# Kernel tuning notes

Hardware: AMD Instinct MI355X
Metric: run time of the kernel (lower is better)

Reference implementation:

```python
import jax, jax.numpy as jnp
import numpy as np

TOP_K = 2


def setup_inputs() -> dict:
    key = jax.random.key(0)
    ks = jax.random.split(key, 5)
    B, S, D, F, E = 2, 1024, 1024, 4096, 8
    return {
        "hidden_states": jax.random.normal(ks[0], (B, S, D), jnp.float32),
        "gate_w": jax.random.normal(ks[1], (E, D), jnp.float32) * 0.02,
        "w1": jax.random.normal(ks[2], (E, D, F), jnp.float32) * 0.02,
        "w2": jax.random.normal(ks[3], (E, F, D), jnp.float32) * 0.02,
        "w3": jax.random.normal(ks[4], (E, D, F), jnp.float32) * 0.02,
    }


def reference(hidden_states, gate_w, w1, w2, w3):
    B, S, D = hidden_states.shape
    E = gate_w.shape[0]
    x = hidden_states.reshape(-1, D).astype(jnp.float32)  # [T, D]
    T = x.shape[0]

    # Router: softmax over experts, top-k, renormalize selected weights.
    router_logits = x @ gate_w.T                      # [T, E]
    probs = jax.nn.softmax(router_logits, axis=-1)
    top_w, top_e = jax.lax.top_k(probs, TOP_K)        # [T, K]
    top_w = top_w / jnp.sum(top_w, axis=-1, keepdims=True)

    # Combine weights [T, E]: weight of expert e for token t (0 if not selected).
    combine = jnp.zeros((T, E), jnp.float32).at[jnp.arange(T)[:, None], top_e].add(top_w)

    # Expert SwiGLU FFNs (vectorized over experts; unselected contributions are
    # zeroed by combine weights, matching the gather/scatter math exactly).
    h = jnp.einsum('td,edf->etf', x, w1)              # [E, T, F]
    g = jnp.einsum('td,edf->etf', x, w3)              # [E, T, F]
    y = jnp.einsum('etf,efd->etd', jax.nn.silu(h) * g, w2)  # [E, T, D]

    out = jnp.einsum('etd,te->td', y, combine)        # weighted scatter-combine
    return out.reshape(B, S, D), router_logits
```

## Files before the change

### kernel.cpp

```cpp
#include <hip/hip_runtime.h>
#include <hip/hip_bf16.h>
#include <math.h>

#define T_TOK   2048
#define DDIM    1024
#define FDIM    4096
#define NEXP    8
#define MAXROWS 4608

typedef __bf16          bf16x8 __attribute__((ext_vector_type(8)));
typedef float           f32x4  __attribute__((ext_vector_type(4)));
typedef unsigned short  u16x8  __attribute__((ext_vector_type(8)));

#define LDSP 40
#define FCW  128

static __device__ __forceinline__ unsigned short f2b(float f) {
    __hip_bfloat16 h = __float2bfloat16(f);
    return __builtin_bit_cast(unsigned short, h);
}

static __device__ __forceinline__ void gll16(const unsigned short* g, unsigned short* l) {
    __builtin_amdgcn_global_load_lds(
        (const __attribute__((address_space(1))) unsigned int*)g,
        (__attribute__((address_space(3))) unsigned int*)l, 16, 0, 0);
}

__global__ __launch_bounds__(256) void moe_router_kernel(
    const float* __restrict__ x, const float* __restrict__ gate_w,
    float* __restrict__ logits_out, int* __restrict__ top_e, float* __restrict__ top_w)
{
    int wid  = (blockIdx.x * blockDim.x + threadIdx.x) >> 6;
    int lane = threadIdx.x & 63;
    if (wid >= T_TOK) return;
    const float* xr = x + (size_t)wid * DDIM;
    float acc[NEXP];
    #pragma unroll
    for (int e = 0; e < NEXP; ++e) acc[e] = 0.f;
    for (int d = lane; d < DDIM; d += 64) {
        float xv = xr[d];
        #pragma unroll
        for (int e = 0; e < NEXP; ++e) acc[e] += xv * gate_w[e * DDIM + d];
    }
    #pragma unroll
    for (int e = 0; e < NEXP; ++e) {
        #pragma unroll
        for (int off = 32; off > 0; off >>= 1)
            acc[e] += __shfl_down(acc[e], off, 64);
    }
    if (lane == 0) {
        #pragma unroll
        for (int e = 0; e < NEXP; ++e) logits_out[wid * NEXP + e] = acc[e];
        int e1 = 0;
        #pragma unroll
        for (int e = 1; e < NEXP; ++e) if (acc[e] > acc[e1]) e1 = e;
        int e2 = (e1 == 0) ? 1 : 0;
        #pragma unroll
        for (int e = 0; e < NEXP; ++e) if (e != e1 && acc[e] > acc[e2]) e2 = e;
        float p2 = __expf(acc[e2] - acc[e1]);
        float s  = 1.0f + p2;
        top_e[wid * 2]     = e1;
        top_e[wid * 2 + 1] = e2;
        top_w[wid * 2]     = 1.0f / s;
        top_w[wid * 2 + 1] = p2 / s;
    }
}

__global__ void moe_scatter_kernel(const int* __restrict__ top_e, const float* __restrict__ top_w,
                                   int* __restrict__ cnt, int* __restrict__ list_tok,
                                   float* __restrict__ list_w)
{
    int t = blockIdx.x * blockDim.x + threadIdx.x;
    if (t >= T_TOK) return;
    #pragma unroll
    for (int s = 0; s < 2; ++s) {
        int e   = top_e[t * 2 + s];
        int pos = atomicAdd(&cnt[e], 1);
        list_tok[e * T_TOK + pos] = t;
        list_w [e * T_TOK + pos] = top_w[t * 2 + s];
    }
}

__global__ void moe_prefix_kernel(const int* __restrict__ cnt, int* __restrict__ offs)
{
    if (threadIdx.x == 0 && blockIdx.x == 0) {
        int o = 0;
        #pragma unroll
        for (int e = 0; e < NEXP; ++e) { offs[e] = o; o += ((cnt[e] + 63) >> 6) << 6; }
        offs[NEXP] = o;
    }
}

__global__ __launch_bounds__(256) void transpose_cvt2_kernel(
    const float* __restrict__ srcA, unsigned short* __restrict__ dstA,
    const float* __restrict__ srcB, unsigned short* __restrict__ dstB, int R, int C)
{
    int tilesC = C >> 6;
    int tilesPerMat = (R >> 6) * tilesC;
    int e  = blockIdx.x / tilesPerMat;
    int t  = blockIdx.x - e * tilesPerMat;
    int tr = t / tilesC, tc = t - tr * tilesC;
    size_t soff = (size_t)e * R * C + (size_t)(tr * 64) * C + tc * 64;
    size_t doff = (size_t)e * R * C + (size_t)(tc * 64) * R + tr * 64;

    __shared__ unsigned short lds[64][72];
    int tid = threadIdx.x;
    int rr = tid >> 4, cc = (tid & 15) * 4;
    int orow = tid >> 2, oc = (tid & 3) * 16;

    #pragma unroll
    for (int m = 0; m < 2; ++m) {
        const float*    s = (m == 0 ? srcA : srcB) + soff;
        unsigned short* d = (m == 0 ? dstA : dstB) + doff;
        if (m) __syncthreads();
        #pragma unroll
        for (int i = 0; i < 4; ++i) {
            int r = rr + 16 * i;
            float4 v = *(const float4*)(s + (size_t)r * C + cc);
            lds[cc + 0][r] = f2b(v.x); lds[cc + 1][r] = f2b(v.y);
            lds[cc + 2][r] = f2b(v.z); lds[cc + 3][r] = f2b(v.w);
        }
        __syncthreads();
        u16x8 a = *(const u16x8*)&lds[orow][oc];
        u16x8 b = *(const u16x8*)&lds[orow][oc + 8];
        *(u16x8*)(d + (size_t)orow * R + oc)     = a;
        *(u16x8*)(d + (size_t)orow * R + oc + 8) = b;
    }
}

__global__ __launch_bounds__(256) void transpose_cvt_kernel(
    const float* __restrict__ src, unsigned short* __restrict__ dst, int R, int C)
{
    int tilesC = C >> 6;
    int tilesPerMat = (R >> 6) * tilesC;
    int e  = blockIdx.x / tilesPerMat;
    int t  = blockIdx.x - e * tilesPerMat;
    int tr = t / tilesC, tc = t - tr * tilesC;
    const float*    s = src + (size_t)e * R * C + (size_t)(tr * 64) * C + tc * 64;
    unsigned short* d = dst + (size_t)e * R * C + (size_t)(tc * 64) * R + tr * 64;

    __shared__ unsigned short lds[64][72];
    int tid = threadIdx.x;
    int rr = tid >> 4, cc = (tid & 15) * 4;
    #pragma unroll
    for (int i = 0; i < 4; ++i) {
        int r = rr + 16 * i;
        float4 v = *(const float4*)(s + (size_t)r * C + cc);
        lds[cc + 0][r] = f2b(v.x); lds[cc + 1][r] = f2b(v.y);
        lds[cc + 2][r] = f2b(v.z); lds[cc + 3][r] = f2b(v.w);
    }
    __syncthreads();
    int orow = tid >> 2, oc = (tid & 3) * 16;
    u16x8 a = *(const u16x8*)&lds[orow][oc];
    u16x8 b = *(const u16x8*)&lds[orow][oc + 8];
    *(u16x8*)(d + (size_t)orow * R + oc)     = a;
    *(u16x8*)(d + (size_t)orow * R + oc + 8) = b;
}

__global__ __launch_bounds__(256) void moe_gather_kernel(
    const float* __restrict__ x, const int* __restrict__ list_tok,
    const int* __restrict__ cnt, const int* __restrict__ offs,
    unsigned short* __restrict__ xg)
{
    int e  = blockIdx.x >> 8;
    int rb = blockIdx.x & 255;
    int n = cnt[e];
    int npad = (n + 63) & ~63;
    if (rb * 8 >= npad) return;
    int base = offs[e];
    int tid = threadIdx.x;
    #pragma unroll
    for (int i = 0; i < 4; ++i) {
        int u = tid + 256 * i;
        int r = u >> 7, cu = u & 127;
        int slot = rb * 8 + r;
        int tok = list_tok[e * T_TOK + slot];
        const float* sp = x + (size_t)tok * DDIM + cu * 8;
        float4 v0 = *(const float4*)(sp);
        float4 v1 = *(const float4*)(sp + 4);
        u16x8 t8;
        t8[0]=f2b(v0.x); t8[1]=f2b(v0.y); t8[2]=f2b(v0.z); t8[3]=f2b(v0.w);
        t8[4]=f2b(v1.x); t8[5]=f2b(v1.y); t8[6]=f2b(v1.z); t8[7]=f2b(v1.w);
        *(u16x8*)(xg + (size_t)(base + slot) * DDIM + cu * 8) = t8;
    }
}

__global__ __launch_bounds__(256, 3) void moe_up_kernel(
    const unsigned short* __restrict__ xg,
    const unsigned short* __restrict__ w1t, const unsigned short* __restrict__ w3t,
    const int* __restrict__ cnt, const int* __restrict__ offs,
    unsigned short* __restrict__ act)
{
    int e   = blockIdx.x & 7;
    int idx = blockIdx.x >> 3;
    int mt  = idx >> 6;
    int fc  = idx & 63;
    int n = cnt[e];
    int npad = (n + 63) & ~63;
    if (mt * 128 >= npad) return;
    int rowBase  = offs[e] + mt * 128;
    int rowMax   = offs[e] + npad - 1;
    int rowLimit = offs[e] + npad;

    __shared__ unsigned short As [128 * 32];
    __shared__ unsigned short B1s[64 * 32];
    __shared__ unsigned short B2s[64 * 32];

    int tid = threadIdx.x;
    int lane = tid & 63, wv = tid >> 6;
    int c = lane & 15, g = lane >> 4;
    int wr = (wv >> 1) * 64, wc = (wv & 1) * 32;

    int srow = tid >> 2, skc = tid & 3;
    int r0 = min(rowBase + srow,      rowMax);
    int r1 = min(rowBase + 64 + srow, rowMax);
    const unsigned short* gA0 = xg + (size_t)r0 * DDIM + skc * 8;
    const unsigned short* gA1 = xg + (size_t)r1 * DDIM + skc * 8;
    size_t wb = (size_t)e * FDIM * DDIM + (size_t)(fc * 64 + srow) * DDIM + skc * 8;
    const unsigned short* gB1 = w1t + wb;
    const unsigned short* gB2 = w3t + wb;
    unsigned short* lA0 = As  + tid * 8;
    unsigned short* lA1 = As  + 2048 + tid * 8;
    unsigned short* lB1 = B1s + tid * 8;
    unsigned short* lB2 = B2s + tid * 8;

    f32x4 acc_h[4][2], acc_g[4][2];
    #pragma unroll
    for (int i = 0; i < 4; ++i)
        #pragma unroll
        for (int j = 0; j < 2; ++j) { acc_h[i][j] = (f32x4)(0.f); acc_g[i][j] = (f32x4)(0.f); }

    for (int k0 = 0; k0 < DDIM; k0 += 32) {
        gll16(gA0 + k0, lA0);
        gll16(gA1 + k0, lA1);
        gll16(gB1 + k0, lB1);
        gll16(gB2 + k0, lB2);
        __syncthreads();

        bf16x8 af[4];
        #pragma unroll
        for (int mi = 0; mi < 4; ++mi)
            af[mi] = *reinterpret_cast<const bf16x8*>(&As[(wr + mi * 16 + c) * 32 + g * 8]);
        #pragma unroll
        for (int ni = 0; ni < 2; ++ni) {
            bf16x8 b1 = *reinterpret_cast<const bf16x8*>(&B1s[(wc + ni * 16 + c) * 32 + g * 8]);
            bf16x8 b2 = *reinterpret_cast<const bf16x8*>(&B2s[(wc + ni * 16 + c) * 32 + g * 8]);
            #pragma unroll
            for (int mi = 0; mi < 4; ++mi) {
                acc_h[mi][ni] = __builtin_amdgcn_mfma_f32_16x16x32_bf16(af[mi], b1, acc_h[mi][ni], 0, 0, 0);
                acc_g[mi][ni] = __builtin_amdgcn_mfma_f32_16x16x32_bf16(af[mi], b2, acc_g[mi][ni], 0, 0, 0);
            }
        }
        __syncthreads();
    }

    #pragma unroll
    for (int mi = 0; mi < 4; ++mi) {
        int row = rowBase + wr + mi * 16 + 4 * g;
        if (row < rowLimit) {
            #pragma unroll
            for (int ni = 0; ni < 2; ++ni) {
                int col = fc * 64 + wc + ni * 16 + c;
                #pragma unroll
                for (int r = 0; r < 4; ++r) {
                    float h  = acc_h[mi][ni][r];
                    float gg = acc_g[mi][ni][r];
                    float a  = h / (1.f + __expf(-h)) * gg;
                    act[(size_t)(row + r) * FDIM + col] = f2b(a);
                }
            }
        }
    }
}

__global__ __launch_bounds__(256, 4) void moe_down_kernel(
    const unsigned short* __restrict__ act, const unsigned short* __restrict__ w2t,
    const int* __restrict__ cnt, const int* __restrict__ offs,
    const int* __restrict__ list_tok, const float* __restrict__ list_w,
    float* __restrict__ out)
{
    int e   = blockIdx.x & 7;
    int idx = blockIdx.x >> 3;
    int mt  = idx >> 5;
    int ks  = (idx >> 4) & 1;
    int dc  = idx & 15;
    int n = cnt[e];
    int npad = (n + 63) & ~63;
    if (mt * 128 >= npad) return;
    int rowBase = offs[e] + mt * 128;
    int rowMax  = offs[e] + npad - 1;

    __shared__ unsigned short As[128 * 32];
    __shared__ unsigned short Bs[64 * 32];

    int tid = threadIdx.x;
    int lane = tid & 63, wv = tid >> 6;
    int c = lane & 15, g = lane >> 4;
    int wr = (wv >> 1) * 64, wc = (wv & 1) * 32;

    int srow = tid >> 2, skc = tid & 3;
    int r0 = min(rowBase + srow,      rowMax);
    int r1 = min(rowBase + 64 + srow, rowMax);
    const unsigned short* gA0 = act + (size_t)r0 * FDIM + ks * 2048 + skc * 8;
    const unsigned short* gA1 = act + (size_t)r1 * FDIM + ks * 2048 + skc * 8;
    const unsigned short* gB  = w2t + (size_t)e * DDIM * FDIM
                                    + (size_t)(dc * 64 + srow) * FDIM + ks * 2048 + skc * 8;
    unsigned short* lA0 = As + tid * 8;
    unsigned short* lA1 = As + 2048 + tid * 8;
    unsigned short* lB  = Bs + tid * 8;

    f32x4 acc[4][2];
    #pragma unroll
    for (int i = 0; i < 4; ++i)
        #pragma unroll
        for (int j = 0; j < 2; ++j) acc[i][j] = (f32x4)(0.f);

    for (int k0 = 0; k0 < 2048; k0 += 32) {
        gll16(gA0 + k0, lA0);
        gll16(gA1 + k0, lA1);
        gll16(gB  + k0, lB);
        __syncthreads();

        bf16x8 af[4];
        #pragma unroll
        for (int mi = 0; mi < 4; ++mi)
            af[mi] = *reinterpret_cast<const bf16x8*>(&As[(wr + mi * 16 + c) * 32 + g * 8]);
        #pragma unroll
        for (int ni = 0; ni < 2; ++ni) {
            bf16x8 b = *reinterpret_cast<const bf16x8*>(&Bs[(wc + ni * 16 + c) * 32 + g * 8]);
            #pragma unroll
            for (int mi = 0; mi < 4; ++mi)
                acc[mi][ni] = __builtin_amdgcn_mfma_f32_16x16x32_bf16(af[mi], b, acc[mi][ni], 0, 0, 0);
        }
        __syncthreads();
    }

    #pragma unroll
    for (int mi = 0; mi < 4; ++mi) {
        #pragma unroll
        for (int r = 0; r < 4; ++r) {
            int s = mt * 128 + wr + mi * 16 + 4 * g + r;
            if (s < n) {
                int   tok = list_tok[e * T_TOK + s];
                float wt  = list_w [e * T_TOK + s];
                #pragma unroll
                for (int ni = 0; ni < 2; ++ni) {
                    int col = dc * 64 + wc + ni * 16 + c;
                    atomicAdd(&out[(size_t)tok * DDIM + col], wt * acc[mi][ni][r]);
                }
            }
        }
    }
}

__global__ __launch_bounds__(256, 3) void moe_up_legacy(
    const float* __restrict__ x, const float* __restrict__ w1, const float* __restrict__ w3,
    const int* __restrict__ cnt, const int* __restrict__ offs,
    const int* __restrict__ list_tok, unsigned short* __restrict__ act)
{
    const int NWG = NEXP * 32 * 32;
    int bid     = blockIdx.x;
    int logical = (bid & 7) * (NWG >> 3) + (bid >> 3);
    int tile = logical & 31;
    int fc   = (logical >> 5) & 31;
    int e    = logical >> 10;
    int n = cnt[e];
    if (tile * 64 >= n) return;

    __shared__ unsigned short As [64  * LDSP];
    __shared__ unsigned short B1s[FCW * LDSP];
    __shared__ unsigned short B2s[FCW * LDSP];

    int tid = threadIdx.x;
    int lane = tid & 63, wv = tid >> 6;
    int c = lane & 15, g = lane >> 4;
    int ar = tid >> 2, akq = tid & 3;
    int tok = list_tok[e * T_TOK + tile * 64 + ar];
    const float* xrow = x + (size_t)tok * DDIM + akq * 8;
    int bcol = tid & 127, bkh = tid >> 7;
    const size_t wbase = (size_t)e * DDIM * FDIM + (size_t)fc * FCW + bcol;
    const float* w1c = w1 + wbase;
    const float* w3c = w3 + wbase;

    f32x4 acc_h[4][2], acc_g[4][2];
    #pragma unroll
    for (int i = 0; i < 4; ++i)
        #pragma unroll
        for (int j = 0; j < 2; ++j) { acc_h[i][j] = (f32x4)(0.f); acc_g[i][j] = (f32x4)(0.f); }

    for (int k0 = 0; k0 < DDIM; k0 += 32) {
        {
            const float4 v0 = *(const float4*)(xrow + k0);
            const float4 v1 = *(const float4*)(xrow + k0 + 4);
            u16x8 t8;
            t8[0]=f2b(v0.x); t8[1]=f2b(v0.y); t8[2]=f2b(v0.z); t8[3]=f2b(v0.w);
            t8[4]=f2b(v1.x); t8[5]=f2b(v1.y); t8[6]=f2b(v1.z); t8[7]=f2b(v1.w);
            *reinterpret_cast<u16x8*>(&As[ar * LDSP + akq * 8]) = t8;
        }
        {
            int kb = k0 + bkh * 16;
            u16x8 t1a, t1b, t2a, t2b;
            #pragma unroll
            for (int j = 0; j < 8; ++j) {
                t1a[j] = f2b(w1c[(size_t)(kb + j)     * FDIM]);
                t1b[j] = f2b(w1c[(size_t)(kb + 8 + j) * FDIM]);
                t2a[j] = f2b(w3c[(size_t)(kb + j)     * FDIM]);
                t2b[j] = f2b(w3c[(size_t)(kb + 8 + j) * FDIM]);
            }
            *reinterpret_cast<u16x8*>(&B1s[bcol * LDSP + bkh * 16])     = t1a;
            *reinterpret_cast<u16x8*>(&B1s[bcol * LDSP + bkh * 16 + 8]) = t1b;
            *reinterpret_cast<u16x8*>(&B2s[bcol * LDSP + bkh * 16])     = t2a;
            *reinterpret_cast<u16x8*>(&B2s[bcol * LDSP + bkh * 16 + 8]) = t2b;
        }
        __syncthreads();
        bf16x8 af[4];
        #pragma unroll
        for (int mi = 0; mi < 4; ++mi)
            af[mi] = *reinterpret_cast<const bf16x8*>(&As[(mi * 16 + c) * LDSP + g * 8]);
        #pragma unroll
        for (int ni = 0; ni < 2; ++ni) {
            int col = wv * 32 + ni * 16 + c;
            bf16x8 b1 = *reinterpret_cast<const bf16x8*>(&B1s[col * LDSP + g * 8]);
            bf16x8 b2 = *reinterpret_cast<const bf16x8*>(&B2s[col * LDSP + g * 8]);
            #pragma unroll
            for (int mi = 0; mi < 4; ++mi) {
                acc_h[mi][ni] = __builtin_amdgcn_mfma_f32_16x16x32_bf16(af[mi], b1, acc_h[mi][ni], 0, 0, 0);
                acc_g[mi][ni] = __builtin_amdgcn_mfma_f32_16x16x32_bf16(af[mi], b2, acc_g[mi][ni], 0, 0, 0);
            }
        }
        __syncthreads();
    }
    int rowBase = offs[e] + tile * 64;
    #pragma unroll
    for (int mi = 0; mi < 4; ++mi)
        #pragma unroll
        for (int ni = 0; ni < 2; ++ni)
            #pragma unroll
            for (int r = 0; r < 4; ++r) {
                float h  = acc_h[mi][ni][r];
                float gg = acc_g[mi][ni][r];
                float a  = h / (1.f + __expf(-h)) * gg;
                int row = rowBase + mi * 16 + 4 * g + r;
                int col = fc * FCW + wv * 32 + ni * 16 + c;
                act[(size_t)row * FDIM + col] = f2b(a);
            }
}

__global__ __launch_bounds__(256, 3) void moe_down_legacy(
    const unsigned short* __restrict__ act, const float* __restrict__ w2,
    const int* __restrict__ cnt, const int* __restrict__ offs,
    const int* __restrict__ list_tok, const float* __restrict__ list_w,
    float* __restrict__ out)
{
    const int NWG = NEXP * 4 * 4 * 32;
    int bid     = blockIdx.x;
    int logical = (bid & 7) * (NWG >> 3) + (bid >> 3);
    int tile = logical & 31;
    int ks   = (logical >> 5) & 3;
    int dc   = (logical >> 7) & 3;
    int e    = logical >> 9;
    int n = cnt[e];
    if (tile * 64 >= n) return;

    __shared__ unsigned short As[64  * LDSP];
    __shared__ unsigned short Bs[256 * LDSP];
    int tid = threadIdx.x;
    int lane = tid & 63, wv = tid >> 6;
    int c = lane & 15, g = lane >> 4;
    int rowBase = offs[e] + tile * 64;
    int ar = tid >> 2, akq = tid & 3;
    const unsigned short* arow = act + (size_t)(rowBase + ar) * FDIM + ks * 1024 + akq * 8;
    const float* w2c = w2 + (size_t)e * FDIM * DDIM + (size_t)(ks * 1024) * DDIM + (size_t)dc * 256 + tid;

    f32x4 acc[4][4];
    #pragma unroll
    for (int i = 0; i < 4; ++i)
        #pragma unroll
        for (int j = 0; j < 4; ++j) acc[i][j] = (f32x4)(0.f);

    for (int k0 = 0; k0 < 1024; k0 += 32) {
        *reinterpret_cast<u16x8*>(&As[ar * LDSP + akq * 8]) = *reinterpret_cast<const u16x8*>(arow + k0);
        #pragma unroll
        for (int kk = 0; kk < 4; ++kk) {
            u16x8 t1;
            #pragma unroll
            for (int j = 0; j < 8; ++j)
                t1[j] = f2b(w2c[(size_t)(k0 + kk * 8 + j) * DDIM]);
            *reinterpret_cast<u16x8*>(&Bs[tid * LDSP + kk * 8]) = t1;
        }
        __syncthreads();
        bf16x8 af[4];
        #pragma unroll
        for (int mi = 0; mi < 4; ++mi)
            af[mi] = *reinterpret_cast<const bf16x8*>(&As[(mi * 16 + c) * LDSP + g * 8]);
        #pragma unroll
        for (int ni = 0; ni < 4; ++ni) {
            bf16x8 b = *reinterpret_cast<const bf16x8*>(&Bs[(wv * 64 + ni * 16 + c) * LDSP + g * 8]);
            #pragma unroll
            for (int mi = 0; mi < 4; ++mi)
                acc[mi][ni] = __builtin_amdgcn_mfma_f32_16x16x32_bf16(af[mi], b, acc[mi][ni], 0, 0, 0);
        }
        __syncthreads();
    }
    #pragma unroll
    for (int mi = 0; mi < 4; ++mi)
        #pragma unroll
        for (int r = 0; r < 4; ++r) {
            int s = tile * 64 + mi * 16 + 4 * g + r;
            if (s < n) {
                int   tok = list_tok[e * T_TOK + s];
                float wt  = list_w [e * T_TOK + s];
                #pragma unroll
                for (int ni = 0; ni < 4; ++ni) {
                    int col = dc * 256 + wv * 64 + ni * 16 + c;
                    atomicAdd(&out[(size_t)tok * DDIM + col], wt * acc[mi][ni][r]);
                }
            }
        }
}

extern "C" void kernel_launch(void* const* d_in, const int* in_sizes, int n_in,
                              void* d_out, int out_size, void* d_ws, size_t ws_size,
                              hipStream_t stream) {
    const float* x      = (const float*)d_in[0];
    const float* gate_w = (const float*)d_in[1];
    const float* w1     = (const float*)d_in[2];
    const float* w2     = (const float*)d_in[3];
    const float* w3     = (const float*)d_in[4];
    float* out        = (float*)d_out;
    float* logits_out = out + (size_t)T_TOK * DDIM;

    char* ws = (char*)d_ws;
    int*   cnt      = (int*)  (ws);
    int*   offs     = (int*)  (ws + 64);
    int*   top_e    = (int*)  (ws + 1024);
    float* top_w    = (float*)(ws + 17408);
    int*   list_tok = (int*)  (ws + 33792);
    float* list_w   = (float*)(ws + 99328);

    hipMemsetAsync(cnt, 0, 64, stream);
    hipMemsetAsync(list_tok, 0, 131072, stream);
    hipMemsetAsync(out, 0, (size_t)T_TOK * DDIM * sizeof(float), stream);

    moe_router_kernel <<<T_TOK / 4,   256, 0, stream>>>(x, gate_w, logits_out, top_e, top_w);
    moe_scatter_kernel<<<T_TOK / 256, 256, 0, stream>>>(top_e, top_w, cnt, list_tok, list_w);
    moe_prefix_kernel <<<1, 64, 0, stream>>>(cnt, offs);

    const size_t MB = 1u << 20;
    const size_t NEED = 241 * MB;
    if (ws_size >= NEED) {
        unsigned short* xg  = (unsigned short*)(ws + 1   * MB);
        unsigned short* act = (unsigned short*)(ws + 11  * MB);
        unsigned short* w1t = (unsigned short*)(ws + 49  * MB);
        unsigned short* w3t = (unsigned short*)(ws + 113 * MB);
        unsigned short* w2t = (unsigned short*)(ws + 177 * MB);

        moe_gather_kernel<<<NEXP * 256, 256, 0, stream>>>(x, list_tok, cnt, offs, xg);
        transpose_cvt2_kernel<<<NEXP * 16 * 64, 256, 0, stream>>>(w1, w1t, w3, w3t, DDIM, FDIM);
        transpose_cvt_kernel <<<NEXP * 64 * 16, 256, 0, stream>>>(w2, w2t, FDIM, DDIM);

        moe_up_kernel   <<<NEXP * 16 * 64, 256, 0, stream>>>(xg, w1t, w3t, cnt, offs, act);
        moe_down_kernel <<<NEXP * 16 * 32, 256, 0, stream>>>(act, w2t, cnt, offs, list_tok, list_w, out);
    } else {
        unsigned short* act = (unsigned short*)(ws + 164864);
        moe_up_legacy   <<<NEXP * 32 * 32,    256, 0, stream>>>(x, w1, w3, cnt, offs, list_tok, act);
        moe_down_legacy <<<NEXP * 4 * 4 * 32, 256, 0, stream>>>(act, w2, cnt, offs, list_tok, list_w, out);
    }
}
```

Before: 355.7 us.

## Fuse weight transpose and bf16 conversion into MoE GEMM tile loads

Removes the separate transpose/convert kernels for w1, w3 and w2 and instead loads fp32 weights directly inside the up and down GEMMs, converting to bf16 and packing into swizzled LDS tiles. Block index ordering is changed so M tiles sharing a weight tile are adjacent, to improve L2 reuse of weights. The down kernel uses a wider 128-column tile with a 4-way K split, and XOR swizzles are added for LDS bank conflicts. The trade-off is synchronous fp32 global loads in the inner loop and repeated weight reads per M tile, instead of a one-time bf16 pre-pass.

```diff
diff --git a/kernel.cpp b/kernel.cpp
--- a/kernel.cpp
+++ b/kernel.cpp
@@ -6,7 +6,6 @@
 #define DDIM    1024
 #define FDIM    4096
 #define NEXP    8
-#define MAXROWS 4608
 
 typedef __bf16          bf16x8 __attribute__((ext_vector_type(8)));
 typedef float           f32x4  __attribute__((ext_vector_type(4)));
@@ -91,72 +90,6 @@
     }
 }
 
-__global__ __launch_bounds__(256) void transpose_cvt2_kernel(
-    const float* __restrict__ srcA, unsigned short* __restrict__ dstA,
-    const float* __restrict__ srcB, unsigned short* __restrict__ dstB, int R, int C)
-{
-    int tilesC = C >> 6;
-    int tilesPerMat = (R >> 6) * tilesC;
-    int e  = blockIdx.x / tilesPerMat;
-    int t  = blockIdx.x - e * tilesPerMat;
-    int tr = t / tilesC, tc = t - tr * tilesC;
-    size_t soff = (size_t)e * R * C + (size_t)(tr * 64) * C + tc * 64;
-    size_t doff = (size_t)e * R * C + (size_t)(tc * 64) * R + tr * 64;
-
-    __shared__ unsigned short lds[64][72];
-    int tid = threadIdx.x;
-    int rr = tid >> 4, cc = (tid & 15) * 4;
-    int orow = tid >> 2, oc = (tid & 3) * 16;
-
-    #pragma unroll
-    for (int m = 0; m < 2; ++m) {
-        const float*    s = (m == 0 ? srcA : srcB) + soff;
-        unsigned short* d = (m == 0 ? dstA : dstB) + doff;
-        if (m) __syncthreads();
-        #pragma unroll
-        for (int i = 0; i < 4; ++i) {
-            int r = rr + 16 * i;
-            float4 v = *(const float4*)(s + (size_t)r * C + cc);
-            lds[cc + 0][r] = f2b(v.x); lds[cc + 1][r] = f2b(v.y);
-            lds[cc + 2][r] = f2b(v.z); lds[cc + 3][r] = f2b(v.w);
-        }
-        __syncthreads();
-        u16x8 a = *(const u16x8*)&lds[orow][oc];
-        u16x8 b = *(const u16x8*)&lds[orow][oc + 8];
-        *(u16x8*)(d + (size_t)orow * R + oc)     = a;
-        *(u16x8*)(d + (size_t)orow * R + oc + 8) = b;
-    }
-}
-
-__global__ __launch_bounds__(256) void transpose_cvt_kernel(
-    const float* __restrict__ src, unsigned short* __restrict__ dst, int R, int C)
-{
-    int tilesC = C >> 6;
-    int tilesPerMat = (R >> 6) * tilesC;
-    int e  = blockIdx.x / tilesPerMat;
-    int t  = blockIdx.x - e * tilesPerMat;
-    int tr = t / tilesC, tc = t - tr * tilesC;
-    const float*    s = src + (size_t)e * R * C + (size_t)(tr * 64) * C + tc * 64;
-    unsigned short* d = dst + (size_t)e * R * C + (size_t)(tc * 64) * R + tr * 64;
-
-    __shared__ unsigned short lds[64][72];
-    int tid = threadIdx.x;
-    int rr = tid >> 4, cc = (tid & 15) * 4;
-    #pragma unroll
-    for (int i = 0; i < 4; ++i) {
-        int r = rr + 16 * i;
-        float4 v = *(const float4*)(s + (size_t)r * C + cc);
-        lds[cc + 0][r] = f2b(v.x); lds[cc + 1][r] = f2b(v.y);
-        lds[cc + 2][r] = f2b(v.z); lds[cc + 3][r] = f2b(v.w);
-    }
-    __syncthreads();
-    int orow = tid >> 2, oc = (tid & 3) * 16;
-    u16x8 a = *(const u16x8*)&lds[orow][oc];
-    u16x8 b = *(const u16x8*)&lds[orow][oc + 8];
-    *(u16x8*)(d + (size_t)orow * R + oc)     = a;
-    *(u16x8*)(d + (size_t)orow * R + oc + 8) = b;
-}
-
 __global__ __launch_bounds__(256) void moe_gather_kernel(
     const float* __restrict__ x, const int* __restrict__ list_tok,
     const int* __restrict__ cnt, const int* __restrict__ offs,
@@ -176,25 +109,25 @@
         int slot = rb * 8 + r;
         int tok = list_tok[e * T_TOK + slot];
         const float* sp = x + (size_t)tok * DDIM + cu * 8;
-        float4 v0 = *(const float4*)(sp);
-        float4 v1 = *(const float4*)(sp + 4);
+        f32x4 v0 = *(const f32x4*)(sp);
+        f32x4 v1 = *(const f32x4*)(sp + 4);
         u16x8 t8;
-        t8[0]=f2b(v0.x); t8[1]=f2b(v0.y); t8[2]=f2b(v0.z); t8[3]=f2b(v0.w);
-        t8[4]=f2b(v1.x); t8[5]=f2b(v1.y); t8[6]=f2b(v1.z); t8[7]=f2b(v1.w);
+        t8[0]=f2b(v0[0]); t8[1]=f2b(v0[1]); t8[2]=f2b(v0[2]); t8[3]=f2b(v0[3]);
+        t8[4]=f2b(v1[0]); t8[5]=f2b(v1[1]); t8[6]=f2b(v1[2]); t8[7]=f2b(v1[3]);
         *(u16x8*)(xg + (size_t)(base + slot) * DDIM + cu * 8) = t8;
     }
 }
 
 __global__ __launch_bounds__(256, 3) void moe_up_kernel(
     const unsigned short* __restrict__ xg,
-    const unsigned short* __restrict__ w1t, const unsigned short* __restrict__ w3t,
+    const float* __restrict__ w1, const float* __restrict__ w3,
     const int* __restrict__ cnt, const int* __restrict__ offs,
     unsigned short* __restrict__ act)
 {
     int e   = blockIdx.x & 7;
     int idx = blockIdx.x >> 3;
-    int mt  = idx >> 6;
-    int fc  = idx & 63;
+    int fc  = idx >> 4;
+    int mt  = idx & 15;
     int n = cnt[e];
     int npad = (n + 63) & ~63;
     if (mt * 128 >= npad) return;
@@ -212,17 +145,23 @@
     int wr = (wv >> 1) * 64, wc = (wv & 1) * 32;
 
     int srow = tid >> 2, skc = tid & 3;
+    int skcs = skc ^ ((srow >> 1) & 3);
     int r0 = min(rowBase + srow,      rowMax);
     int r1 = min(rowBase + 64 + srow, rowMax);
-    const unsigned short* gA0 = xg + (size_t)r0 * DDIM + skc * 8;
-    const unsigned short* gA1 = xg + (size_t)r1 * DDIM + skc * 8;
-    size_t wb = (size_t)e * FDIM * DDIM + (size_t)(fc * 64 + srow) * DDIM + skc * 8;
-    const unsigned short* gB1 = w1t + wb;
-    const unsigned short* gB2 = w3t + wb;
-    unsigned short* lA0 = As  + tid * 8;
-    unsigned short* lA1 = As  + 2048 + tid * 8;
-    unsigned short* lB1 = B1s + tid * 8;
-    unsigned short* lB2 = B2s + tid * 8;
+    const unsigned short* gA0 = xg + (size_t)r0 * DDIM + skcs * 8;
+    const unsigned short* gA1 = xg + (size_t)r1 * DDIM + skcs * 8;
+    unsigned short* lA0 = As + tid * 8;
+    unsigned short* lA1 = As + 2048 + tid * 8;
+
+    int f4 = (tid & 15) * 4;
+    int kp = tid >> 4;
+    const float* gW1 = w1 + (size_t)e * DDIM * FDIM + (size_t)(2 * kp) * FDIM + fc * 64 + f4;
+    const float* gW3 = w3 + (size_t)e * DDIM * FDIM + (size_t)(2 * kp) * FDIM + fc * 64 + f4;
+    int bg   = (kp >> 2) ^ ((f4 >> 2) & 3);
+    int wOff = f4 * 32 + bg * 8 + (kp & 3) * 2;
+
+    int gA = g ^ ((c >> 1) & 3);
+    int gB = g ^ (c >> 2);
 
     f32x4 acc_h[4][2], acc_g[4][2];
     #pragma unroll
@@ -233,18 +172,30 @@
     for (int k0 = 0; k0 < DDIM; k0 += 32) {
         gll16(gA0 + k0, lA0);
         gll16(gA1 + k0, lA1);
-        gll16(gB1 + k0, lB1);
-        gll16(gB2 + k0, lB2);
+        {
+            f32x4 v0 = *(const f32x4*)(gW1 + (size_t)k0 * FDIM);
+            f32x4 v1 = *(const f32x4*)(gW1 + (size_t)(k0 + 1) * FDIM);
+            f32x4 u0 = *(const f32x4*)(gW3 + (size_t)k0 * FDIM);
+            f32x4 u1 = *(const f32x4*)(gW3 + (size_t)(k0 + 1) * FDIM);
+            #pragma unroll
+            for (int j = 0; j < 4; ++j) {
+                unsigned int p1 = (unsigned int)f2b(v0[j]) | ((unsigned int)f2b(v1[j]) << 16);
+                unsigned int p2 = (unsigned int)f2b(u0[j]) | ((unsigned int)f2b(u1[j]) << 16);
+                *(unsigned int*)&B1s[wOff + j * 32] = p1;
+                *(unsigned int*)&B2s[wOff + j * 32] = p2;
+            }
+        }
         __syncthreads();
 
         bf16x8 af[4];
         #pragma unroll
         for (int mi = 0; mi < 4; ++mi)
-            af[mi] = *reinterpret_cast<const bf16x8*>(&As[(wr + mi * 16 + c) * 32 + g * 8]);
+            af[mi] = *reinterpret_cast<const bf16x8*>(&As[(wr + mi * 16 + c) * 32 + gA * 8]);
         #pragma unroll
         for (int ni = 0; ni < 2; ++ni) {
-            bf16x8 b1 = *reinterpret_cast<const bf16x8*>(&B1s[(wc + ni * 16 + c) * 32 + g * 8]);
-            bf16x8 b2 = *reinterpret_cast<const bf16x8*>(&B2s[(wc + ni * 16 + c) * 32 + g * 8]);
+            int col = wc + ni * 16 + c;
+            bf16x8 b1 = *reinterpret_cast<const bf16x8*>(&B1s[col * 32 + gB * 8]);
+            bf16x8 b2 = *reinterpret_cast<const bf16x8*>(&B2s[col * 32 + gB * 8]);
             #pragma unroll
             for (int mi = 0; mi < 4; ++mi) {
                 acc_h[mi][ni] = __builtin_amdgcn_mfma_f32_16x16x32_bf16(af[mi], b1, acc_h[mi][ni], 0, 0, 0);
@@ -273,17 +224,18 @@
     }
 }
 
-__global__ __launch_bounds__(256, 4) void moe_down_kernel(
-    const unsigned short* __restrict__ act, const unsigned short* __restrict__ w2t,
+__global__ __launch_bounds__(256, 3) void moe_down_kernel(
+    const unsigned short* __restrict__ act, const float* __restrict__ w2,
     const int* __restrict__ cnt, const int* __restrict__ offs,
     const int* __restrict__ list_tok, const float* __restrict__ list_w,
     float* __restrict__ out)
 {
     int e   = blockIdx.x & 7;
     int idx = blockIdx.x >> 3;
-    int mt  = idx >> 5;
-    int ks  = (idx >> 4) & 1;
-    int dc  = idx & 15;
+    int dk  = idx >> 4;
+    int mt  = idx & 15;
+    int ks  = dk >> 3;
+    int dc  = dk & 7;
     int n = cnt[e];
     int npad = (n + 63) & ~63;
     if (mt * 128 >= npad) return;
@@ -291,43 +243,67 @@
     int rowMax  = offs[e] + npad - 1;
 
     __shared__ unsigned short As[128 * 32];
-    __shared__ unsigned short Bs[64 * 32];
+    __shared__ unsigned short Bs[128 * 32];
 
     int tid = threadIdx.x;
     int lane = tid & 63, wv = tid >> 6;
     int c = lane & 15, g = lane >> 4;
-    int wr = (wv >> 1) * 64, wc = (wv & 1) * 32;
+    int wr = (wv >> 1) * 64, wc = (wv & 1) * 64;
 
     int srow = tid >> 2, skc = tid & 3;
+    int skcs = skc ^ ((srow >> 1) & 3);
     int r0 = min(rowBase + srow,      rowMax);
     int r1 = min(rowBase + 64 + srow, rowMax);
-    const unsigned short* gA0 = act + (size_t)r0 * FDIM + ks * 2048 + skc * 8;
-    const unsigned short* gA1 = act + (size_t)r1 * FDIM + ks * 2048 + skc * 8;
-    const unsigned short* gB  = w2t + (size_t)e * DDIM * FDIM
-                                    + (size_t)(dc * 64 + srow) * FDIM + ks * 2048 + skc * 8;
+    const unsigned short* gA0 = act + (size_t)r0 * FDIM + ks * 1024 + skcs * 8;
+    const unsigned short* gA1 = act + (size_t)r1 * FDIM + ks * 1024 + skcs * 8;
     unsigned short* lA0 = As + tid * 8;
     unsigned short* lA1 = As + 2048 + tid * 8;
-    unsigned short* lB  = Bs + tid * 8;
-
-    f32x4 acc[4][2];
+
+    int d4  = (tid & 31) * 4;
+    int kpb = tid >> 5;
+    const float* gW2 = w2 + (size_t)e * FDIM * DDIM
+                          + (size_t)(ks * 1024 + 2 * kpb) * DDIM + dc * 128 + d4;
+    int bq = (d4 >> 2) & 3;
+    int bg0   = (kpb >> 2) ^ bq;
+    int bg1   = (((kpb + 8) >> 2)) ^ bq;
+    int wOff0 = d4 * 32 + bg0 * 8 + (kpb & 3) * 2;
+    int wOff1 = d4 * 32 + bg1 * 8 + ((kpb + 8) & 3) * 2;
+
+    int gAs = g ^ ((c >> 1) & 3);
+    int gB  = g ^ (c >> 2);
+
+    f32x4 acc[4][4];
     #pragma unroll
     for (int i = 0; i < 4; ++i)
         #pragma unroll
-        for (int j = 0; j < 2; ++j) acc[i][j] = (f32x4)(0.f);
-
-    for (int k0 = 0; k0 < 2048; k0 += 32) {
+        for (int j = 0; j < 4; ++j) acc[i][j] = (f32x4)(0.f);
+
+    for (int k0 = 0; k0 < 1024; k0 += 32) {
         gll16(gA0 + k0, lA0);
         gll16(gA1 + k0, lA1);
-        gll16(gB  + k0, lB);
+        {
+            f32x4 v0 = *(const f32x4*)(gW2 + (size_t)k0 * DDIM);
+            f32x4 v1 = *(const f32x4*)(gW2 + (size_t)(k0 + 1) * DDIM);
+            f32x4 u0 = *(const f32x4*)(gW2 + (size_t)(k0 + 16) * DDIM);
+            f32x4 u1 = *(const f32x4*)(gW2 + (size_t)(k0 + 17) * DDIM);
+            #pragma unroll
+            for (int j = 0; j < 4; ++j) {
+                unsigned int p0 = (unsigned int)f2b(v0[j]) | ((unsigned int)f2b(v1[j]) << 16);
+                unsigned int p1 = (unsigned int)f2b(u0[j]) | ((unsigned int)f2b(u1[j]) << 16);
+                *(unsigned int*)&Bs[wOff0 + j * 32] = p0;
+                *(unsigned int*)&Bs[wOff1 + j * 32] = p1;
+            }
+        }
         __syncthreads();
 
         bf16x8 af[4];
         #pragma unroll
         for (int mi = 0; mi < 4; ++mi)
-            af[mi] = *reinterpret_cast<const bf16x8*>(&As[(wr + mi * 16 + c) * 32 + g * 8]);
-        #pragma unroll
-        for (int ni = 0; ni < 2; ++ni) {
-            bf16x8 b = *reinterpret_cast<const bf16x8*>(&Bs[(wc + ni * 16 + c) * 32 + g * 8]);
+            af[mi] = *reinterpret_cast<const bf16x8*>(&As[(wr + mi * 16 + c) * 32 + gAs * 8]);
+        #pragma unroll
+        for (int ni = 0; ni < 4; ++ni) {
+            int col = wc + ni * 16 + c;
+            bf16x8 b = *reinterpret_cast<const bf16x8*>(&Bs[col * 32 + gB * 8]);
             #pragma unroll
             for (int mi = 0; mi < 4; ++mi)
                 acc[mi][ni] = __builtin_amdgcn_mfma_f32_16x16x32_bf16(af[mi], b, acc[mi][ni], 0, 0, 0);
@@ -344,8 +320,8 @@
                 int   tok = list_tok[e * T_TOK + s];
                 float wt  = list_w [e * T_TOK + s];
                 #pragma unroll
-                for (int ni = 0; ni < 2; ++ni) {
-                    int col = dc * 64 + wc + ni * 16 + c;
+                for (int ni = 0; ni < 4; ++ni) {
+                    int col = dc * 128 + wc + ni * 16 + c;
                     atomicAdd(&out[(size_t)tok * DDIM + col], wt * acc[mi][ni][r]);
                 }
             }
@@ -547,20 +523,14 @@
     moe_prefix_kernel <<<1, 64, 0, stream>>>(cnt, offs);
 
     const size_t MB = 1u << 20;
-    const size_t NEED = 241 * MB;
+    const size_t NEED = 49 * MB;
     if (ws_size >= NEED) {
-        unsigned short* xg  = (unsigned short*)(ws + 1   * MB);
-        unsigned short* act = (unsigned short*)(ws + 11  * MB);
-        unsigned short* w1t = (unsigned short*)(ws + 49  * MB);
-        unsigned short* w3t = (unsigned short*)(ws + 113 * MB);
-        unsigned short* w2t = (unsigned short*)(ws + 177 * MB);
+        unsigned short* xg  = (unsigned short*)(ws + 1  * MB);
+        unsigned short* act = (unsigned short*)(ws + 11 * MB);
 
         moe_gather_kernel<<<NEXP * 256, 256, 0, stream>>>(x, list_tok, cnt, offs, xg);
-        transpose_cvt2_kernel<<<NEXP * 16 * 64, 256, 0, stream>>>(w1, w1t, w3, w3t, DDIM, FDIM);
-        transpose_cvt_kernel <<<NEXP * 64 * 16, 256, 0, stream>>>(w2, w2t, FDIM, DDIM);
-
-        moe_up_kernel   <<<NEXP * 16 * 64, 256, 0, stream>>>(xg, w1t, w3t, cnt, offs, act);
-        moe_down_kernel <<<NEXP * 16 * 32, 256, 0, stream>>>(act, w2t, cnt, offs, list_tok, list_w, out);
+        moe_up_kernel   <<<NEXP * 16 * 64, 256, 0, stream>>>(xg, w1, w3, cnt, offs, act);
+        moe_down_kernel <<<NEXP * 16 * 32, 256, 0, stream>>>(act, w2, cnt, offs, list_tok, list_w, out);
     } else {
         unsigned short* act = (unsigned short*)(ws + 164864);
         moe_up_legacy   <<<NEXP * 32 * 32,    256, 0, stream>>>(x, w1, w3, cnt, offs, list_tok, act);
```

Result: slower. 384.5 us (+8.1%).
